# Kernel tuning notes

Hardware: AMD Instinct MI355X
Metric: run time of the kernel (lower is better)

Reference implementation:

```python
import jax, jax.numpy as jnp
import numpy as np

N, E, S, T, B, F = 50000, 150000, 32, 32, 64, 3
R = 1.1


def setup_inputs() -> dict:
    key = jax.random.key(0)
    k1, k2, k3, k4 = jax.random.split(key, 4)
    x = jax.random.normal(k1, (N, F), dtype=jnp.float32)
    # direction vectors, columns normalized (as in torch init)
    v = jax.random.uniform(k2, (T, F), dtype=jnp.float32) - 0.5
    v = (v / jnp.sqrt(jnp.sum(v * v, axis=1, keepdims=True))).T  # [F, T]
    lin = jnp.linspace(-R, R, S, dtype=jnp.float32)  # [S]
    edge_index = jax.random.randint(k3, (2, E), 0, N, dtype=jnp.int64)
    batch = jnp.sort(jax.random.randint(k4, (N,), 0, B, dtype=jnp.int64))
    return {"x": x, "v": v, "lin": lin, "edge_index": edge_index,
            "batch": batch, "num_graphs": B}


def _ecc_sum(h, idx, lin, num_graphs):
    # h: [M, T] heights, idx: [M] graph ids, lin: [S]
    # bump: sigmoid(50 * (lin - h)) -> [M, S, T]
    e = jax.nn.sigmoid(50.0 * (lin[None, :, None] - h[:, None, :]))
    return jax.ops.segment_sum(e, idx, num_segments=num_graphs)  # [B, S, T]


def reference(x, v, lin, edge_index, batch, num_graphs):
    nh = x @ v                                # [N, T] node heights
    eh = jnp.max(nh[edge_index], axis=0)      # [E, T] edge heights (max over endpoints)
    node_ect = _ecc_sum(nh, batch, lin, num_graphs)
    edge_ect = _ecc_sum(eh, batch[edge_index[0]], lin, num_graphs)
    return node_ect - edge_ect                # [B, S, T] == movedim(0,1) layout of torch
```

## Files before the change

### kernel.cpp

```cpp
#include <hip/hip_runtime.h>

#ifndef __has_builtin
#define __has_builtin(x) 0
#endif

__device__ __forceinline__ float fexp2(float x) {
#if __has_builtin(__builtin_amdgcn_exp2f)
    return __builtin_amdgcn_exp2f(x);
#else
    return exp2f(x);
#endif
}
__device__ __forceinline__ float frcp(float x) {
#if __has_builtin(__builtin_amdgcn_rcpf)
    return __builtin_amdgcn_rcpf(x);
#else
    return 1.0f / x;
#endif
}

constexpr int TT = 32;
constexpr int SS = 32;
constexpr int BB = 64;
constexpr int NB = 64;
constexpr int CPB_N = 8;
constexpr int CPB_E = 32;
constexpr float FL = 50.0f * 1.44269504088896340736f;
constexpr float QS = 65536.0f;
constexpr float IQS = 1.0f / 65536.0f;

__global__ __launch_bounds__(256) void prep_k(
    const int* __restrict__ batch, const int* __restrict__ src,
    int N, int E, int nB,
    int* __restrict__ starts, int* __restrict__ hist, float* __restrict__ out)
{
    if ((int)blockIdx.x < nB) {
        const int n = blockIdx.x * 256 + threadIdx.x;
        if (n >= N) return;
        const int g = batch[n];
        const int gp = (n == 0) ? -1 : batch[n - 1];
        for (int g2 = gp + 1; g2 <= g; ++g2) starts[g2] = n;
        if (n == N - 1)
            for (int g2 = g + 1; g2 <= BB; ++g2) starts[g2] = N;
    } else {
        const int b = blockIdx.x - nB;
        float4* o4 = (float4*)(out + (size_t)b * SS * TT);
        o4[threadIdx.x] = float4{0.f, 0.f, 0.f, 0.f};
        __shared__ int h[BB];
        if (threadIdx.x < BB) h[threadIdx.x] = 0;
        __syncthreads();
        const int per = (E + NB - 1) / NB;
        const int lo = b * per, hi = min(E, lo + per);
        for (int e = lo + threadIdx.x; e < hi; e += 256)
            atomicAdd(&h[batch[src[e]]], 1);
        __syncthreads();
        if (threadIdx.x < BB) hist[b * BB + threadIdx.x] = h[threadIdx.x];
    }
}

__global__ __launch_bounds__(256) void scatter_k(
    const int* __restrict__ src, const int* __restrict__ dst,
    const int* __restrict__ batch, int E,
    const int* __restrict__ hist,
    int* __restrict__ offs, int* __restrict__ ssrc, int* __restrict__ sdst)
{
    __shared__ int lcur[BB];
    __shared__ int stot[BB];
    const int tid = threadIdx.x;
    if (tid < BB) {
        int accb = 0, tot = 0;
        for (int b = 0; b < NB; ++b) {
            const int hv = hist[b * BB + tid];
            accb += (b < (int)blockIdx.x) ? hv : 0;
            tot += hv;
        }
        lcur[tid] = accb;
        stot[tid] = tot;
    }
    __syncthreads();
    if (tid == 0) {
        int run = 0;
        for (int i = 0; i < BB; ++i) { const int tv = stot[i]; stot[i] = run; run += tv; }
        if (blockIdx.x == 0) offs[BB] = run;
    }
    __syncthreads();
    if (tid < BB) {
        lcur[tid] += stot[tid];
        if (blockIdx.x == 0) offs[tid] = stot[tid];
    }
    __syncthreads();
    const int per = (E + NB - 1) / NB;
    const int lo = blockIdx.x * per, hi = min(E, lo + per);
    for (int e = lo + tid; e < hi; e += 256) {
        const int s = src[e], d = dst[e];
        const int pos = atomicAdd(&lcur[batch[s]], 1);
        ssrc[pos] = s;
        sdst[pos] = d;
    }
}

__global__ __launch_bounds__(256) void ect_k(
    const float* __restrict__ x, const float* __restrict__ v,
    const float* __restrict__ lin,
    const int* __restrict__ ssrc, const int* __restrict__ sdst,
    const int* __restrict__ starts, const int* __restrict__ offs,
    float* __restrict__ out)
{
    __shared__ unsigned accS[TT][SS + 1];
    __shared__ unsigned cntS[TT][SS + 1];
    for (int i = threadIdx.x; i < TT * (SS + 1); i += 256) {
        ((unsigned*)accS)[i] = 0u;
        ((unsigned*)cntS)[i] = 0u;
    }

    const bool edge = blockIdx.x >= BB * CPB_N;
    const int bid = edge ? blockIdx.x - BB * CPB_N : blockIdx.x;
    const int CPB = edge ? CPB_E : CPB_N;
    const int g = bid / CPB;
    const int c = bid % CPB;
    const int* bnds = edge ? offs : starts;
    const int s0 = bnds[g], s1 = bnds[g + 1];
    const int chunk = (s1 - s0 + CPB - 1) / CPB;
    const int lo = s0 + c * chunk;
    const int hi = min(s1, lo + chunk);

    const int t = threadIdx.x & 31;
    const int pr = threadIdx.x >> 5;
    const float v0 = v[t], v1 = v[TT + t], v2 = v[2 * TT + t];
    const float l0 = lin[0];
    const float dS = lin[1] - l0;
    const float invD = frcp(dS);
    const float fld = FL * dS;
    const float pm2 = fexp2(2.f * fld), pm1 = fexp2(fld);
    const float pp1 = fexp2(-fld), pp2 = fexp2(-2.f * fld);
    __syncthreads();

#pragma unroll 2
    for (int base = lo; base < hi; base += 8) {
        const int p = base + pr;
        if (p < hi) {
            float h;
            if (edge) {
                const int sn = ssrc[p], dn = sdst[p];
                const float hs = fmaf(x[3 * sn], v0, fmaf(x[3 * sn + 1], v1, x[3 * sn + 2] * v2));
                const float hd = fmaf(x[3 * dn], v0, fmaf(x[3 * dn + 1], v1, x[3 * dn + 2] * v2));
                h = fmaxf(hs, hd);
            } else {
                h = fmaf(x[3 * p], v0, fmaf(x[3 * p + 1], v1, x[3 * p + 2] * v2));
            }
            const float hl0 = h - l0;
            float fj = rintf(hl0 * invD);
            fj = fminf(34.f, fmaxf(-3.f, fj));
            const int j = (int)fj;
            const float delta = fmaf(-fj, dS, hl0);
            const float ucen = fexp2(FL * delta);
            unsigned q[5];
            q[0] = (unsigned)__float2uint_rn(QS * frcp(fmaf(ucen, pm2, 1.f)));
            q[1] = (unsigned)__float2uint_rn(QS * frcp(fmaf(ucen, pm1, 1.f)));
            q[2] = (unsigned)__float2uint_rn(QS * frcp(1.f + ucen));
            q[3] = (unsigned)__float2uint_rn(QS * frcp(fmaf(ucen, pp1, 1.f)));
            q[4] = (unsigned)__float2uint_rn(QS * frcp(fmaf(ucen, pp2, 1.f)));
            const int b = j + 3;
            if (b < SS) atomicAdd(&cntS[t][b], 1u);
#pragma unroll
            for (int m = 0; m < 5; ++m) {
                const int s = j - 2 + m;
                if (0 <= s && s < SS) atomicAdd(&accS[t][s], q[m]);
            }
        }
    }
    __syncthreads();
    float* cval = (float*)cntS;
    if (threadIdx.x < TT) {
        const int tt = threadIdx.x;
        unsigned run = 0u;
#pragma unroll
        for (int s = 0; s < SS; ++s) {
            run += cntS[tt][s];
            const float vfull = fmaf((float)accS[tt][s], IQS, (float)run);
            cval[tt * (SS + 1) + s] = vfull;
        }
    }
    __syncthreads();
    const float sign = edge ? -1.f : 1.f;
    float* o = out + (size_t)g * SS * TT;
#pragma unroll
    for (int k = 0; k < 4; ++k) {
        const int s = 4 * pr + k;
        atomicAdd(&o[s * TT + t], sign * cval[t * (SS + 1) + s]);
    }
}

extern "C" void kernel_launch(void* const* d_in, const int* in_sizes, int n_in,
                              void* d_out, int out_size, void* d_ws, size_t ws_size,
                              hipStream_t stream) {
    const float* x   = (const float*)d_in[0];
    const float* v   = (const float*)d_in[1];
    const float* lin = (const float*)d_in[2];
    const int* edge_index = (const int*)d_in[3];
    const int* batch = (const int*)d_in[4];

    const int N = in_sizes[0] / 3;
    const int E = in_sizes[3] / 2;
    const int* src = edge_index;
    const int* dst = edge_index + E;
    float* out = (float*)d_out;

    char* ws = (char*)d_ws;
    int* starts = (int*)ws;
    int* offs   = (int*)(ws + 512);
    int* hist   = (int*)(ws + 1024);
    int* ssrc   = (int*)(ws + 65536);
    int* sdst   = ssrc + E;

    const int nB = (N + 255) / 256;
    prep_k<<<nB + NB, 256, 0, stream>>>(batch, src, N, E, nB, starts, hist, out);
    scatter_k<<<NB, 256, 0, stream>>>(src, dst, batch, E, hist, offs, ssrc, sdst);
    ect_k<<<BB * (CPB_N + CPB_E), 256, 0, stream>>>(x, v, lin, ssrc, sdst, starts, offs, out);
}
```

Baseline: 37.63 us.

## Overlap node ECT with edge scatter and trim sigmoid taps to three

Node-height ECT work now runs in the same launch as the edge scatter, so the node half overlaps the scatter instead of waiting for the edge sort. Edge ECT runs in its own kernel with half as many chunks per graph. The per-element sigmoid stencil drops from five quantized taps to three, which cuts exp/rcp work and shared atomics. The cumulative count is computed by a parallel partial scan across warps instead of one serial thread. Fewer taps rely on the steep sigmoid saturating within one bin, so accuracy near bin edges is slightly lower.

```diff
diff --git a/kernel.cpp b/kernel.cpp
--- a/kernel.cpp
+++ b/kernel.cpp
@@ -24,7 +24,7 @@
 constexpr int BB = 64;
 constexpr int NB = 64;
 constexpr int CPB_N = 8;
-constexpr int CPB_E = 32;
+constexpr int CPB_E = 16;
 constexpr float FL = 50.0f * 1.44269504088896340736f;
 constexpr float QS = 65536.0f;
 constexpr float IQS = 1.0f / 65536.0f;
@@ -58,72 +58,19 @@
     }
 }
 
-__global__ __launch_bounds__(256) void scatter_k(
-    const int* __restrict__ src, const int* __restrict__ dst,
-    const int* __restrict__ batch, int E,
-    const int* __restrict__ hist,
-    int* __restrict__ offs, int* __restrict__ ssrc, int* __restrict__ sdst)
-{
-    __shared__ int lcur[BB];
-    __shared__ int stot[BB];
-    const int tid = threadIdx.x;
-    if (tid < BB) {
-        int accb = 0, tot = 0;
-        for (int b = 0; b < NB; ++b) {
-            const int hv = hist[b * BB + tid];
-            accb += (b < (int)blockIdx.x) ? hv : 0;
-            tot += hv;
-        }
-        lcur[tid] = accb;
-        stot[tid] = tot;
-    }
-    __syncthreads();
-    if (tid == 0) {
-        int run = 0;
-        for (int i = 0; i < BB; ++i) { const int tv = stot[i]; stot[i] = run; run += tv; }
-        if (blockIdx.x == 0) offs[BB] = run;
-    }
-    __syncthreads();
-    if (tid < BB) {
-        lcur[tid] += stot[tid];
-        if (blockIdx.x == 0) offs[tid] = stot[tid];
-    }
-    __syncthreads();
-    const int per = (E + NB - 1) / NB;
-    const int lo = blockIdx.x * per, hi = min(E, lo + per);
-    for (int e = lo + tid; e < hi; e += 256) {
-        const int s = src[e], d = dst[e];
-        const int pos = atomicAdd(&lcur[batch[s]], 1);
-        ssrc[pos] = s;
-        sdst[pos] = d;
-    }
-}
-
-__global__ __launch_bounds__(256) void ect_k(
+__device__ __forceinline__ void ect_core(
     const float* __restrict__ x, const float* __restrict__ v,
     const float* __restrict__ lin,
     const int* __restrict__ ssrc, const int* __restrict__ sdst,
-    const int* __restrict__ starts, const int* __restrict__ offs,
-    float* __restrict__ out)
+    bool edge, int lo, int hi, int g, float sign, float* __restrict__ out)
 {
     __shared__ unsigned accS[TT][SS + 1];
     __shared__ unsigned cntS[TT][SS + 1];
+    __shared__ unsigned part[TT][9];
     for (int i = threadIdx.x; i < TT * (SS + 1); i += 256) {
         ((unsigned*)accS)[i] = 0u;
         ((unsigned*)cntS)[i] = 0u;
     }
-
-    const bool edge = blockIdx.x >= BB * CPB_N;
-    const int bid = edge ? blockIdx.x - BB * CPB_N : blockIdx.x;
-    const int CPB = edge ? CPB_E : CPB_N;
-    const int g = bid / CPB;
-    const int c = bid % CPB;
-    const int* bnds = edge ? offs : starts;
-    const int s0 = bnds[g], s1 = bnds[g + 1];
-    const int chunk = (s1 - s0 + CPB - 1) / CPB;
-    const int lo = s0 + c * chunk;
-    const int hi = min(s1, lo + chunk);
-
     const int t = threadIdx.x & 31;
     const int pr = threadIdx.x >> 5;
     const float v0 = v[t], v1 = v[TT + t], v2 = v[2 * TT + t];
@@ -131,11 +78,10 @@
     const float dS = lin[1] - l0;
     const float invD = frcp(dS);
     const float fld = FL * dS;
-    const float pm2 = fexp2(2.f * fld), pm1 = fexp2(fld);
-    const float pp1 = fexp2(-fld), pp2 = fexp2(-2.f * fld);
-    __syncthreads();
-
-#pragma unroll 2
+    const float pm1 = fexp2(fld), pp1 = fexp2(-fld);
+    __syncthreads();
+
+#pragma unroll 4
     for (int base = lo; base < hi; base += 8) {
         const int p = base + pr;
         if (p < hi) {
@@ -150,45 +96,110 @@
             }
             const float hl0 = h - l0;
             float fj = rintf(hl0 * invD);
-            fj = fminf(34.f, fmaxf(-3.f, fj));
+            fj = fminf(34.f, fmaxf(-2.f, fj));
             const int j = (int)fj;
             const float delta = fmaf(-fj, dS, hl0);
             const float ucen = fexp2(FL * delta);
-            unsigned q[5];
-            q[0] = (unsigned)__float2uint_rn(QS * frcp(fmaf(ucen, pm2, 1.f)));
-            q[1] = (unsigned)__float2uint_rn(QS * frcp(fmaf(ucen, pm1, 1.f)));
-            q[2] = (unsigned)__float2uint_rn(QS * frcp(1.f + ucen));
-            q[3] = (unsigned)__float2uint_rn(QS * frcp(fmaf(ucen, pp1, 1.f)));
-            q[4] = (unsigned)__float2uint_rn(QS * frcp(fmaf(ucen, pp2, 1.f)));
-            const int b = j + 3;
+            const unsigned q0 = __float2uint_rn(QS * frcp(fmaf(ucen, pm1, 1.f)));
+            const unsigned q1 = __float2uint_rn(QS * frcp(1.f + ucen));
+            const unsigned q2 = __float2uint_rn(QS * frcp(fmaf(ucen, pp1, 1.f)));
+            const int b = j + 2;
             if (b < SS) atomicAdd(&cntS[t][b], 1u);
+            if (1 <= j && j <= SS) atomicAdd(&accS[t][j - 1], q0);
+            if (0 <= j && j < SS)  atomicAdd(&accS[t][j], q1);
+            if (-1 <= j && j < SS - 1) atomicAdd(&accS[t][j + 1], q2);
+        }
+    }
+    __syncthreads();
+    const unsigned c0 = cntS[t][4 * pr], c1 = cntS[t][4 * pr + 1];
+    const unsigned c2 = cntS[t][4 * pr + 2], c3 = cntS[t][4 * pr + 3];
+    part[t][pr + 1] = c0 + c1 + c2 + c3;
+    if (pr == 0) part[t][0] = 0u;
+    __syncthreads();
+    if (pr == 0) {
+        unsigned r = 0u;
 #pragma unroll
-            for (int m = 0; m < 5; ++m) {
-                const int s = j - 2 + m;
-                if (0 <= s && s < SS) atomicAdd(&accS[t][s], q[m]);
+        for (int q = 1; q <= 8; ++q) { r += part[t][q]; part[t][q] = r; }
+    }
+    __syncthreads();
+    unsigned run = part[t][pr];
+    float* o = out + (size_t)g * SS * TT;
+    run += c0;
+    atomicAdd(&o[(4 * pr + 0) * TT + t], sign * fmaf((float)accS[t][4 * pr + 0], IQS, (float)run));
+    run += c1;
+    atomicAdd(&o[(4 * pr + 1) * TT + t], sign * fmaf((float)accS[t][4 * pr + 1], IQS, (float)run));
+    run += c2;
+    atomicAdd(&o[(4 * pr + 2) * TT + t], sign * fmaf((float)accS[t][4 * pr + 2], IQS, (float)run));
+    run += c3;
+    atomicAdd(&o[(4 * pr + 3) * TT + t], sign * fmaf((float)accS[t][4 * pr + 3], IQS, (float)run));
+}
+
+__global__ __launch_bounds__(256) void mid_k(
+    const float* __restrict__ x, const float* __restrict__ v,
+    const float* __restrict__ lin,
+    const int* __restrict__ src, const int* __restrict__ dst,
+    const int* __restrict__ batch, int E,
+    const int* __restrict__ hist, int* __restrict__ offs,
+    int* __restrict__ ssrc, int* __restrict__ sdst,
+    const int* __restrict__ starts, float* __restrict__ out)
+{
+    if ((int)blockIdx.x < NB) {
+        __shared__ int lcur[BB];
+        __shared__ int stot[BB];
+        const int tid = threadIdx.x;
+        if (tid < BB) {
+            int accb = 0, tot = 0;
+            for (int b = 0; b < NB; ++b) {
+                const int hv = hist[b * BB + tid];
+                accb += (b < (int)blockIdx.x) ? hv : 0;
+                tot += hv;
             }
-        }
-    }
-    __syncthreads();
-    float* cval = (float*)cntS;
-    if (threadIdx.x < TT) {
-        const int tt = threadIdx.x;
-        unsigned run = 0u;
-#pragma unroll
-        for (int s = 0; s < SS; ++s) {
-            run += cntS[tt][s];
-            const float vfull = fmaf((float)accS[tt][s], IQS, (float)run);
-            cval[tt * (SS + 1) + s] = vfull;
-        }
-    }
-    __syncthreads();
-    const float sign = edge ? -1.f : 1.f;
-    float* o = out + (size_t)g * SS * TT;
-#pragma unroll
-    for (int k = 0; k < 4; ++k) {
-        const int s = 4 * pr + k;
-        atomicAdd(&o[s * TT + t], sign * cval[t * (SS + 1) + s]);
-    }
+            lcur[tid] = accb;
+            stot[tid] = tot;
+        }
+        __syncthreads();
+        if (tid == 0) {
+            int run = 0;
+            for (int i = 0; i < BB; ++i) { const int tv = stot[i]; stot[i] = run; run += tv; }
+            if (blockIdx.x == 0) offs[BB] = run;
+        }
+        __syncthreads();
+        if (tid < BB) {
+            lcur[tid] += stot[tid];
+            if (blockIdx.x == 0) offs[tid] = stot[tid];
+        }
+        __syncthreads();
+        const int per = (E + NB - 1) / NB;
+        const int lo = blockIdx.x * per, hi = min(E, lo + per);
+        for (int e = lo + tid; e < hi; e += 256) {
+            const int s = src[e], d = dst[e];
+            const int pos = atomicAdd(&lcur[batch[s]], 1);
+            ssrc[pos] = s;
+            sdst[pos] = d;
+        }
+    } else {
+        const int bid = blockIdx.x - NB;
+        const int g = bid / CPB_N, c = bid % CPB_N;
+        const int s0 = starts[g], s1 = starts[g + 1];
+        const int chunk = (s1 - s0 + CPB_N - 1) / CPB_N;
+        const int lo = s0 + c * chunk;
+        const int hi = min(s1, lo + chunk);
+        ect_core(x, v, lin, nullptr, nullptr, false, lo, hi, g, 1.0f, out);
+    }
+}
+
+__global__ __launch_bounds__(256) void edge_k(
+    const float* __restrict__ x, const float* __restrict__ v,
+    const float* __restrict__ lin,
+    const int* __restrict__ ssrc, const int* __restrict__ sdst,
+    const int* __restrict__ offs, float* __restrict__ out)
+{
+    const int g = blockIdx.x / CPB_E, c = blockIdx.x % CPB_E;
+    const int s0 = offs[g], s1 = offs[g + 1];
+    const int chunk = (s1 - s0 + CPB_E - 1) / CPB_E;
+    const int lo = s0 + c * chunk;
+    const int hi = min(s1, lo + chunk);
+    ect_core(x, v, lin, ssrc, sdst, true, lo, hi, g, -1.0f, out);
 }
 
 extern "C" void kernel_launch(void* const* d_in, const int* in_sizes, int n_in,
@@ -215,6 +226,7 @@
 
     const int nB = (N + 255) / 256;
     prep_k<<<nB + NB, 256, 0, stream>>>(batch, src, N, E, nB, starts, hist, out);
-    scatter_k<<<NB, 256, 0, stream>>>(src, dst, batch, E, hist, offs, ssrc, sdst);
-    ect_k<<<BB * (CPB_N + CPB_E), 256, 0, stream>>>(x, v, lin, ssrc, sdst, starts, offs, out);
-}
+    mid_k<<<NB + BB * CPB_N, 256, 0, stream>>>(x, v, lin, src, dst, batch, E,
+                                               hist, offs, ssrc, sdst, starts, out);
+    edge_k<<<BB * CPB_E, 256, 0, stream>>>(x, v, lin, ssrc, sdst, offs, out);
+}
```

After: 34.33 us. -8.8%, faster.
